# Kernel optimization log

Hardware: AMD Instinct MI355X
Metric: run time of the kernel (lower is better)

The kernel has to match this reference:

```python
import jax, jax.numpy as jnp
import numpy as np

N = 50000   # nodes
E = 600000  # edges (time_feat is per-edge: same mask indexes k and src_idx)
D = 128     # adapter_dim
C = 8       # num_clusters
SCALE = D ** -0.5


def setup_inputs() -> dict:
    key = jax.random.key(0)
    ks = jax.random.split(key, 12)
    s = 1.0 / np.sqrt(D)
    return {
        "node_feat": jax.random.normal(ks[0], (N, D), jnp.float32),
        "time_feat": jax.random.normal(ks[1], (E, D), jnp.float32),
        "context_feat": jax.random.normal(ks[2], (N, D), jnp.float32),
        "edge_index": jax.random.randint(ks[3], (2, E), 0, N),
        "Wq": jax.random.uniform(ks[4], (D, D), jnp.float32, -s, s),
        "bq": jnp.zeros((D,), jnp.float32),
        "Wk": jax.random.uniform(ks[5], (D, D), jnp.float32, -s, s),
        "bk": jnp.zeros((D,), jnp.float32),
        "Wv": jax.random.uniform(ks[6], (D, D), jnp.float32, -s, s),
        "bv": jnp.zeros((D,), jnp.float32),
        "cluster_emb": jax.random.normal(ks[7], (C, D), jnp.float32),
        "Wo": jax.random.uniform(ks[8], (D, D), jnp.float32, -s, s),
        "bo": jnp.zeros((D,), jnp.float32),
    }


def reference(node_feat, time_feat, context_feat, edge_index,
              Wq, bq, Wk, bk, Wv, bv, cluster_emb, Wo, bo):
    q = node_feat @ Wq + bq            # [N, D]
    k = time_feat @ Wk + bk            # [E, D]
    v = time_feat @ Wv + bv            # [E, D]

    # cluster routing: argmax(softmax(sim)) == argmax(sim)
    sim = (time_feat @ cluster_emb.T) * SCALE   # [E, C]
    assign = jnp.argmax(sim, axis=-1)           # [E] int

    src = edge_index[0]                          # [E]
    seg = assign * N + src                       # combined (cluster, dst-of-scatter) segment id
    nseg = C * N

    attn = jnp.sum(q[src] * k, axis=-1) * SCALE  # [E]

    # scatter_softmax per (cluster, src node)
    seg_max = jax.ops.segment_max(attn, seg, num_segments=nseg)
    ex = jnp.exp(attn - seg_max[seg])
    denom = jax.ops.segment_sum(ex, seg, num_segments=nseg)
    w = ex / denom[seg]                          # [E]

    # scatter_mean per (cluster, src node) -> [C, N, D]
    wv = v * w[:, None]
    sums = jax.ops.segment_sum(wv, seg, num_segments=nseg)                 # [C*N, D]
    counts = jax.ops.segment_sum(jnp.ones((E,), v.dtype), seg, num_segments=nseg)
    means = sums / jnp.maximum(counts, 1.0)[:, None]                       # empty -> 0
    per_cluster = means.reshape(C, N, D)

    # sum(outputs) / len(outputs): only non-empty clusters contribute an entry
    edges_per_cluster = jax.ops.segment_sum(jnp.ones((E,), jnp.float32), assign, num_segments=C)
    num_nonempty = jnp.sum((edges_per_cluster > 0).astype(jnp.float32))
    combined = per_cluster.sum(axis=0) / num_nonempty                      # [N, D]

    return jax.nn.relu(combined @ Wo + bo)
```

## Files before the change

### kernel.cpp

```cpp
#include <hip/hip_runtime.h>
#include <math.h>


#define NN 50000
#define NE 600000
#define DD 128
#define NC 8
#define SCALEF 0.08838834764831845f

#define OFF_DENOM    0
#define OFF_CNTSEG   400000
#define OFF_NODECNT  800000
#define OFF_FILL     850000
#define OFF_HIST     900000
#define ZERO_ELEMS   900016
#define OFF_NODEOFF  900016
#define OFF_PARTIAL  950016
#define OFF_INVNNE   950272
#define OFF_C0       950276
#define OFF_BQK      950528
#define OFF_BVO      950656
#define OFF_WQBK     950784
#define OFF_WQK      950912
#define OFF_WVO      967296
#define OFF_QB       983680
#define OFF_EX       1033680
#define OFF_ASSIGN   1633680
#define OFF_SORTED   2233680
#define OFF_SW       2833680
#define OFF_P        2883680

__global__ __launch_bounds__(128) void k_pre(
    const float* __restrict__ Wq, const float* __restrict__ bq,
    const float* __restrict__ Wk, const float* __restrict__ bk,
    const float* __restrict__ Wv, const float* __restrict__ bv,
    const float* __restrict__ Wo,
    float* __restrict__ Wqk, float* __restrict__ bqk,
    float* __restrict__ Wvo, float* __restrict__ bvo,
    float* __restrict__ wqbk, float* __restrict__ c0) {
  __shared__ float rq[DD], rv[DD];
  int b = blockIdx.x, i = threadIdx.x;
  if (b < DD) {
    rq[i] = Wq[b * DD + i];
    rv[i] = Wv[b * DD + i];
    __syncthreads();
    float aq = 0.f, av = 0.f;
    for (int j = 0; j < DD; j++) {
      aq += rq[j] * Wk[i * DD + j];
      av += rv[j] * Wo[j * DD + i];
    }
    Wqk[b * DD + i] = aq;
    Wvo[b * DD + i] = av;
  } else {
    float a1 = 0.f, a2 = 0.f, a3 = 0.f;
    for (int j = 0; j < DD; j++) {
      a1 += bq[j] * Wk[i * DD + j];
      a2 += bv[j] * Wo[j * DD + i];
      a3 += Wq[i * DD + j] * bk[j];
    }
    bqk[i] = a1; bvo[i] = a2; wqbk[i] = a3;
    if (i == 0) {
      float s = 0.f;
      for (int j = 0; j < DD; j++) s += bq[j] * bk[j];
      *c0 = s;
    }
  }
}

__global__ __launch_bounds__(256) void k_p(
    const float* __restrict__ nf, const float* __restrict__ Wqk,
    const float* __restrict__ bqk, const float* __restrict__ wqbk,
    const float* __restrict__ c0p,
    float* __restrict__ p, float* __restrict__ qb) {
  __shared__ float a_lds[64 * DD];
  __shared__ float wb_lds[DD];
  int t = threadIdx.x;
  long row0 = (long)blockIdx.x * 64;
  for (int it = 0; it < 8; it++) {
    int idx = (it * 256 + t) * 4;
    long r = row0 + idx / DD;
    float4 v = {0.f, 0.f, 0.f, 0.f};
    if (r < NN) v = *(const float4*)(nf + r * DD + (idx % DD));
    *(float4*)(a_lds + idx) = v;
  }
  if (t < DD) wb_lds[t] = wqbk[t];
  __syncthreads();
  int cg = t % 32, rg = t / 32;
  int col0 = cg * 4, r0 = rg * 8;
  float acc[8][4]; float qacc[8];
  for (int r = 0; r < 8; r++) { qacc[r] = 0.f; for (int c = 0; c < 4; c++) acc[r][c] = 0.f; }
  for (int k = 0; k < DD; k++) {
    float4 b4 = *(const float4*)(Wqk + k * DD + col0);
    float wbk = wb_lds[k];
    for (int r = 0; r < 8; r++) {
      float a = a_lds[(r0 + r) * DD + k];
      acc[r][0] += a * b4.x; acc[r][1] += a * b4.y;
      acc[r][2] += a * b4.z; acc[r][3] += a * b4.w;
      qacc[r] += a * wbk;
    }
  }
  float4 bq4 = *(const float4*)(bqk + col0);
  float c0v = *c0p;
  for (int r = 0; r < 8; r++) {
    long row = row0 + r0 + r;
    if (row < NN) {
      float4 o;
      o.x = acc[r][0] + bq4.x; o.y = acc[r][1] + bq4.y;
      o.z = acc[r][2] + bq4.z; o.w = acc[r][3] + bq4.w;
      *(float4*)(p + row * DD + col0) = o;
      if (cg == 0) qb[row] = qacc[r] + c0v;
    }
  }
}

__global__ __launch_bounds__(256) void k_edge1(
    const float* __restrict__ tf, const int* __restrict__ ei,
    const float* __restrict__ ce, const float* __restrict__ p,
    const float* __restrict__ qb,
    float* __restrict__ denom, int* __restrict__ cnt_seg,
    int* __restrict__ node_cnt, int* __restrict__ hist,
    float* __restrict__ exv, int* __restrict__ assign) {
  __shared__ float ce_lds[NC * DD];
  __shared__ int lhist[NC];
  int t = threadIdx.x;
  if (t < NC) lhist[t] = 0;
  *(float4*)(ce_lds + t * 4) = *(const float4*)(ce + t * 4);
  __syncthreads();

  int el = t >> 2, j = t & 3;
  long e = (long)blockIdx.x * 64 + el;
  const float* trow = tf + e * DD;
  float4 tv[8];
  for (int i = 0; i < 8; i++) tv[i] = *(const float4*)(trow + i * 16 + j * 4);
  int src = ei[e];

  float sims[NC];
  for (int c = 0; c < NC; c++) {
    const float* cr = ce_lds + c * DD;
    float s = 0.f;
    for (int i = 0; i < 8; i++) {
      float4 cv = *(const float4*)(cr + i * 16 + j * 4);
      s += tv[i].x * cv.x + tv[i].y * cv.y + tv[i].z * cv.z + tv[i].w * cv.w;
    }
    sims[c] = s;
  }
  for (int c = 0; c < NC; c++) {
    sims[c] += __shfl_xor(sims[c], 1);
    sims[c] += __shfl_xor(sims[c], 2);
  }
  float best = sims[0]; int bc = 0;
  for (int c = 1; c < NC; c++) if (sims[c] > best) { best = sims[c]; bc = c; }

  const float* prow = p + (long)src * DD;
  float a = 0.f;
  for (int i = 0; i < 8; i++) {
    float4 pv = *(const float4*)(prow + i * 16 + j * 4);
    a += tv[i].x * pv.x + tv[i].y * pv.y + tv[i].z * pv.z + tv[i].w * pv.w;
  }
  a += __shfl_xor(a, 1);
  a += __shfl_xor(a, 2);
  float attn = (a + qb[src]) * SCALEF;
  float ex = expf(attn);

  if (j == 0) {
    exv[e] = ex;
    assign[e] = bc;
    int seg = bc * NN + src;
    atomicAdd(&denom[seg], ex);
    atomicAdd(&cnt_seg[seg], 1);
    atomicAdd(&node_cnt[src], 1);
    atomicAdd(&lhist[bc], 1);
  }
  __syncthreads();
  if (t < NC) atomicAdd(&hist[t], lhist[t]);
}

__global__ __launch_bounds__(256) void k_scan1(const int* __restrict__ node_cnt,
                                               int* __restrict__ partial) {
  int i = blockIdx.x * 256 + threadIdx.x;
  int v = (i < NN) ? node_cnt[i] : 0;
  for (int o = 1; o < 64; o <<= 1) v += __shfl_xor(v, o);
  __shared__ int wsum[4];
  if ((threadIdx.x & 63) == 0) wsum[threadIdx.x >> 6] = v;
  __syncthreads();
  if (threadIdx.x == 0) partial[blockIdx.x] = wsum[0] + wsum[1] + wsum[2] + wsum[3];
}

__global__ __launch_bounds__(256) void k_scan2(int* __restrict__ partial,
                                               const int* __restrict__ hist,
                                               float* __restrict__ inv_nne) {
  __shared__ int s[256];
  int t = threadIdx.x;
  int v = (t < 196) ? partial[t] : 0;
  s[t] = v;
  __syncthreads();
  for (int o = 1; o < 256; o <<= 1) {
    int add = (t >= o) ? s[t - o] : 0;
    __syncthreads();
    s[t] += add;
    __syncthreads();
  }
  if (t < 196) partial[t] = s[t] - v;
  if (t == 0) {
    int nne = 0;
    for (int c = 0; c < NC; c++) nne += (hist[c] > 0) ? 1 : 0;
    *inv_nne = 1.0f / (float)(nne > 0 ? nne : 1);
  }
}

__global__ __launch_bounds__(256) void k_scan3(const int* __restrict__ node_cnt,
                                               const int* __restrict__ partial,
                                               int* __restrict__ node_off) {
  __shared__ int s[256];
  int t = threadIdx.x;
  int i = blockIdx.x * 256 + t;
  int v = (i < NN) ? node_cnt[i] : 0;
  s[t] = v;
  __syncthreads();
  for (int o = 1; o < 256; o <<= 1) {
    int add = (t >= o) ? s[t - o] : 0;
    __syncthreads();
    s[t] += add;
    __syncthreads();
  }
  if (i < NN) node_off[i] = partial[blockIdx.x] + s[t] - v;
}

__global__ __launch_bounds__(256) void k_scatter(const int* __restrict__ ei,
                                                 const int* __restrict__ node_off,
                                                 int* __restrict__ fill,
                                                 int* __restrict__ sorted) {
  long e = (long)blockIdx.x * 256 + threadIdx.x;
  if (e < NE) {
    int s = ei[e];
    int pos = node_off[s] + atomicAdd(&fill[s], 1);
    sorted[pos] = (int)e;
  }
}

__global__ __launch_bounds__(256) void k_edge2(
    const float* __restrict__ tf, const int* __restrict__ sorted,
    const int* __restrict__ node_off, const int* __restrict__ node_cnt,
    const int* __restrict__ assign, const float* __restrict__ exv,
    const float* __restrict__ denom, const int* __restrict__ cnt_seg,
    float* __restrict__ agg, float* __restrict__ sw) {
  int wave = threadIdx.x >> 6, lane = threadIdx.x & 63;
  int n = blockIdx.x * 4 + wave;
  int off = node_off[n], cnt = node_cnt[n];
  float a0 = 0.f, a1 = 0.f, swa = 0.f;
  for (int base = 0; base < cnt; base += 64) {
    int m = cnt - base; if (m > 64) m = 64;
    int e_l = 0; float s_l = 0.f;
    if (lane < m) {
      e_l = sorted[off + base + lane];
      int c = assign[e_l];
      int seg = c * NN + n;
      s_l = exv[e_l] / (denom[seg] * (float)cnt_seg[seg]);
    }
    for (int ii = 0; ii < m; ii++) {
      int e = __shfl(e_l, ii);
      float s = __shfl(s_l, ii);
      float2 tv = *(const float2*)(tf + (long)e * DD + lane * 2);
      a0 += s * tv.x; a1 += s * tv.y; swa += s;
    }
  }
  float2 o; o.x = a0; o.y = a1;
  *(float2*)(agg + (long)n * DD + lane * 2) = o;
  if (lane == 0) sw[n] = swa;
}

__global__ __launch_bounds__(256) void k_out(
    const float* __restrict__ agg, const float* __restrict__ Wvo,
    const float* __restrict__ bvo, const float* __restrict__ sw,
    const float* __restrict__ bo, const float* __restrict__ inv_nne,
    float* __restrict__ out) {
  __shared__ float a_lds[64 * DD];
  __shared__ float sw_lds[64];
  int t = threadIdx.x;
  long row0 = (long)blockIdx.x * 64;
  for (int it = 0; it < 8; it++) {
    int idx = (it * 256 + t) * 4;
    long r = row0 + idx / DD;
    float4 v = {0.f, 0.f, 0.f, 0.f};
    if (r < NN) v = *(const float4*)(agg + r * DD + (idx % DD));
    *(float4*)(a_lds + idx) = v;
  }
  if (t < 64) {
    long r = row0 + t;
    sw_lds[t] = (r < NN) ? sw[r] : 0.f;
  }
  __syncthreads();
  int cg = t % 32, rg = t / 32;
  int col0 = cg * 4, r0 = rg * 8;
  float acc[8][4];
  for (int r = 0; r < 8; r++) for (int c = 0; c < 4; c++) acc[r][c] = 0.f;
  for (int k = 0; k < DD; k++) {
    float4 b4 = *(const float4*)(Wvo + k * DD + col0);
    for (int r = 0; r < 8; r++) {
      float a = a_lds[(r0 + r) * DD + k];
      acc[r][0] += a * b4.x; acc[r][1] += a * b4.y;
      acc[r][2] += a * b4.z; acc[r][3] += a * b4.w;
    }
  }
  float4 bv4 = *(const float4*)(bvo + col0);
  float4 bo4 = *(const float4*)(bo + col0);
  float inv = *inv_nne;
  for (int r = 0; r < 8; r++) {
    long row = row0 + r0 + r;
    if (row < NN) {
      float s = sw_lds[r0 + r];
      float4 o;
      o.x = fmaxf((acc[r][0] + s * bv4.x) * inv + bo4.x, 0.f);
      o.y = fmaxf((acc[r][1] + s * bv4.y) * inv + bo4.y, 0.f);
      o.z = fmaxf((acc[r][2] + s * bv4.z) * inv + bo4.z, 0.f);
      o.w = fmaxf((acc[r][3] + s * bv4.w) * inv + bo4.w, 0.f);
      *(float4*)(out + row * DD + col0) = o;
    }
  }
}

extern "C" void kernel_launch(void* const* d_in, const int* in_sizes, int n_in,
                              void* d_out, int out_size, void* d_ws, size_t ws_size,
                              hipStream_t stream) {
  const float* nf = (const float*)d_in[0];
  const float* tf = (const float*)d_in[1];
  const int*   ei = (const int*)d_in[3];
  const float* Wq = (const float*)d_in[4];
  const float* bq = (const float*)d_in[5];
  const float* Wk = (const float*)d_in[6];
  const float* bk = (const float*)d_in[7];
  const float* Wv = (const float*)d_in[8];
  const float* bv = (const float*)d_in[9];
  const float* ce = (const float*)d_in[10];
  const float* Wo = (const float*)d_in[11];
  const float* bo = (const float*)d_in[12];
  float* out = (float*)d_out;

  float* ws  = (float*)d_ws;
  float* denom    = ws + OFF_DENOM;
  int*   cnt_seg  = (int*)(ws + OFF_CNTSEG);
  int*   node_cnt = (int*)(ws + OFF_NODECNT);
  int*   fill     = (int*)(ws + OFF_FILL);
  int*   hist     = (int*)(ws + OFF_HIST);
  int*   node_off = (int*)(ws + OFF_NODEOFF);
  int*   partial  = (int*)(ws + OFF_PARTIAL);
  float* inv_nne  = ws + OFF_INVNNE;
  float* c0       = ws + OFF_C0;
  float* bqk      = ws + OFF_BQK;
  float* bvo      = ws + OFF_BVO;
  float* wqbk     = ws + OFF_WQBK;
  float* Wqk      = ws + OFF_WQK;
  float* Wvo      = ws + OFF_WVO;
  float* qb       = ws + OFF_QB;
  float* exv      = ws + OFF_EX;
  int*   assign   = (int*)(ws + OFF_ASSIGN);
  int*   sorted   = (int*)(ws + OFF_SORTED);
  float* sw       = ws + OFF_SW;
  float* p        = ws + OFF_P;
  float* agg      = ws + OFF_P;

  hipMemsetAsync(d_ws, 0, (size_t)ZERO_ELEMS * 4, stream);

  k_pre<<<129, 128, 0, stream>>>(Wq, bq, Wk, bk, Wv, bv, Wo, Wqk, bqk, Wvo, bvo, wqbk, c0);
  k_p<<<(NN + 63) / 64, 256, 0, stream>>>(nf, Wqk, bqk, wqbk, c0, p, qb);
  k_edge1<<<NE / 64, 256, 0, stream>>>(tf, ei, ce, p, qb, denom, cnt_seg, node_cnt,
                                       hist, exv, assign);
  k_scan1<<<196, 256, 0, stream>>>(node_cnt, partial);
  k_scan2<<<1, 256, 0, stream>>>(partial, hist, inv_nne);
  k_scan3<<<196, 256, 0, stream>>>(node_cnt, partial, node_off);
  k_scatter<<<(NE + 255) / 256, 256, 0, stream>>>(ei, node_off, fill, sorted);
  k_edge2<<<NN / 4, 256, 0, stream>>>(tf, sorted, node_off, node_cnt, assign, exv,
                                      denom, cnt_seg, agg, sw);
  k_out<<<(NN + 63) / 64, 256, 0, stream>>>(agg, Wvo, bvo, sw, bo, inv_nne, out);
}
```

Measured before the change: 720.2 us.

## Fuse edge scoring into per-node aggregation kernel with LDS-staged time features

Removes the separate per-edge scoring kernel and its global atomics on per-segment denominators and counts. Each node's block now stages its incident time_feat rows in LDS, computes cluster assignment and attention there, and reduces denominators and counts in shared memory. The result is reused for the weighted aggregation, so time_feat is read once instead of twice. Node-degree counting moves into the weight-precompute launch, and the non-empty-cluster count becomes a bitmask OR. The cost is one block per node (50000 blocks) with a slower two-pass chunked path for nodes above 48 edges.

```diff
diff --git a/kernel.cpp b/kernel.cpp
--- a/kernel.cpp
+++ b/kernel.cpp
@@ -6,63 +6,71 @@
 #define NE 600000
 #define DD 128
 #define NC 8
+#define CAP 48
 #define SCALEF 0.08838834764831845f
 
-#define OFF_DENOM    0
-#define OFF_CNTSEG   400000
-#define OFF_NODECNT  800000
-#define OFF_FILL     850000
-#define OFF_HIST     900000
-#define ZERO_ELEMS   900016
-#define OFF_NODEOFF  900016
-#define OFF_PARTIAL  950016
-#define OFF_INVNNE   950272
-#define OFF_C0       950276
-#define OFF_BQK      950528
-#define OFF_BVO      950656
-#define OFF_WQBK     950784
-#define OFF_WQK      950912
-#define OFF_WVO      967296
-#define OFF_QB       983680
-#define OFF_EX       1033680
-#define OFF_ASSIGN   1633680
-#define OFF_SORTED   2233680
-#define OFF_SW       2833680
-#define OFF_P        2883680
-
-__global__ __launch_bounds__(128) void k_pre(
+#define OFF_NODECNT  0
+#define OFF_FILL     50000
+#define OFF_MASK     100000
+#define ZERO_ELEMS   100256
+#define OFF_NODEOFF  100352
+#define OFF_PARTIAL  150352
+#define OFF_BQK      150608
+#define OFF_BVO      150736
+#define OFF_WQBK     150864
+#define OFF_C0       150992
+#define OFF_WQK      151008
+#define OFF_WVO      167392
+#define OFF_QB       183776
+#define OFF_SORTED   233776
+#define OFF_SW       833776
+#define OFF_EXV      883776
+#define OFF_ASSIGN   1483776
+#define OFF_P        2083776
+
+__global__ __launch_bounds__(256) void k_pre_count(
     const float* __restrict__ Wq, const float* __restrict__ bq,
     const float* __restrict__ Wk, const float* __restrict__ bk,
     const float* __restrict__ Wv, const float* __restrict__ bv,
-    const float* __restrict__ Wo,
+    const float* __restrict__ Wo, const int* __restrict__ ei,
+    int* __restrict__ node_cnt,
     float* __restrict__ Wqk, float* __restrict__ bqk,
     float* __restrict__ Wvo, float* __restrict__ bvo,
     float* __restrict__ wqbk, float* __restrict__ c0) {
+  int bid = blockIdx.x, t = threadIdx.x;
+  if (bid >= 129) {
+    long e = (long)(bid - 129) * 256 + t;
+    if (e < NE) atomicAdd(&node_cnt[ei[e]], 1);
+    return;
+  }
   __shared__ float rq[DD], rv[DD];
-  int b = blockIdx.x, i = threadIdx.x;
+  int b = bid;
   if (b < DD) {
-    rq[i] = Wq[b * DD + i];
-    rv[i] = Wv[b * DD + i];
-    __syncthreads();
-    float aq = 0.f, av = 0.f;
-    for (int j = 0; j < DD; j++) {
-      aq += rq[j] * Wk[i * DD + j];
-      av += rv[j] * Wo[j * DD + i];
-    }
-    Wqk[b * DD + i] = aq;
-    Wvo[b * DD + i] = av;
+    if (t < DD) { rq[t] = Wq[b * DD + t]; rv[t] = Wv[b * DD + t]; }
+    __syncthreads();
+    if (t < DD) {
+      float aq = 0.f, av = 0.f;
+      for (int j = 0; j < DD; j++) {
+        aq += rq[j] * Wk[t * DD + j];
+        av += rv[j] * Wo[j * DD + t];
+      }
+      Wqk[b * DD + t] = aq;
+      Wvo[b * DD + t] = av;
+    }
   } else {
-    float a1 = 0.f, a2 = 0.f, a3 = 0.f;
-    for (int j = 0; j < DD; j++) {
-      a1 += bq[j] * Wk[i * DD + j];
-      a2 += bv[j] * Wo[j * DD + i];
-      a3 += Wq[i * DD + j] * bk[j];
-    }
-    bqk[i] = a1; bvo[i] = a2; wqbk[i] = a3;
-    if (i == 0) {
-      float s = 0.f;
-      for (int j = 0; j < DD; j++) s += bq[j] * bk[j];
-      *c0 = s;
+    if (t < DD) {
+      float a1 = 0.f, a2 = 0.f, a3 = 0.f;
+      for (int j = 0; j < DD; j++) {
+        a1 += bq[j] * Wk[t * DD + j];
+        a2 += bv[j] * Wo[j * DD + t];
+        a3 += Wq[t * DD + j] * bk[j];
+      }
+      bqk[t] = a1; bvo[t] = a2; wqbk[t] = a3;
+      if (t == 0) {
+        float s = 0.f;
+        for (int j = 0; j < DD; j++) s += bq[j] * bk[j];
+        *c0 = s;
+      }
     }
   }
 }
@@ -113,68 +121,6 @@
   }
 }
 
-__global__ __launch_bounds__(256) void k_edge1(
-    const float* __restrict__ tf, const int* __restrict__ ei,
-    const float* __restrict__ ce, const float* __restrict__ p,
-    const float* __restrict__ qb,
-    float* __restrict__ denom, int* __restrict__ cnt_seg,
-    int* __restrict__ node_cnt, int* __restrict__ hist,
-    float* __restrict__ exv, int* __restrict__ assign) {
-  __shared__ float ce_lds[NC * DD];
-  __shared__ int lhist[NC];
-  int t = threadIdx.x;
-  if (t < NC) lhist[t] = 0;
-  *(float4*)(ce_lds + t * 4) = *(const float4*)(ce + t * 4);
-  __syncthreads();
-
-  int el = t >> 2, j = t & 3;
-  long e = (long)blockIdx.x * 64 + el;
-  const float* trow = tf + e * DD;
-  float4 tv[8];
-  for (int i = 0; i < 8; i++) tv[i] = *(const float4*)(trow + i * 16 + j * 4);
-  int src = ei[e];
-
-  float sims[NC];
-  for (int c = 0; c < NC; c++) {
-    const float* cr = ce_lds + c * DD;
-    float s = 0.f;
-    for (int i = 0; i < 8; i++) {
-      float4 cv = *(const float4*)(cr + i * 16 + j * 4);
-      s += tv[i].x * cv.x + tv[i].y * cv.y + tv[i].z * cv.z + tv[i].w * cv.w;
-    }
-    sims[c] = s;
-  }
-  for (int c = 0; c < NC; c++) {
-    sims[c] += __shfl_xor(sims[c], 1);
-    sims[c] += __shfl_xor(sims[c], 2);
-  }
-  float best = sims[0]; int bc = 0;
-  for (int c = 1; c < NC; c++) if (sims[c] > best) { best = sims[c]; bc = c; }
-
-  const float* prow = p + (long)src * DD;
-  float a = 0.f;
-  for (int i = 0; i < 8; i++) {
-    float4 pv = *(const float4*)(prow + i * 16 + j * 4);
-    a += tv[i].x * pv.x + tv[i].y * pv.y + tv[i].z * pv.z + tv[i].w * pv.w;
-  }
-  a += __shfl_xor(a, 1);
-  a += __shfl_xor(a, 2);
-  float attn = (a + qb[src]) * SCALEF;
-  float ex = expf(attn);
-
-  if (j == 0) {
-    exv[e] = ex;
-    assign[e] = bc;
-    int seg = bc * NN + src;
-    atomicAdd(&denom[seg], ex);
-    atomicAdd(&cnt_seg[seg], 1);
-    atomicAdd(&node_cnt[src], 1);
-    atomicAdd(&lhist[bc], 1);
-  }
-  __syncthreads();
-  if (t < NC) atomicAdd(&hist[t], lhist[t]);
-}
-
 __global__ __launch_bounds__(256) void k_scan1(const int* __restrict__ node_cnt,
                                                int* __restrict__ partial) {
   int i = blockIdx.x * 256 + threadIdx.x;
@@ -186,9 +132,7 @@
   if (threadIdx.x == 0) partial[blockIdx.x] = wsum[0] + wsum[1] + wsum[2] + wsum[3];
 }
 
-__global__ __launch_bounds__(256) void k_scan2(int* __restrict__ partial,
-                                               const int* __restrict__ hist,
-                                               float* __restrict__ inv_nne) {
+__global__ __launch_bounds__(256) void k_scan2(int* __restrict__ partial) {
   __shared__ int s[256];
   int t = threadIdx.x;
   int v = (t < 196) ? partial[t] : 0;
@@ -201,11 +145,6 @@
     __syncthreads();
   }
   if (t < 196) partial[t] = s[t] - v;
-  if (t == 0) {
-    int nne = 0;
-    for (int c = 0; c < NC; c++) nne += (hist[c] > 0) ? 1 : 0;
-    *inv_nne = 1.0f / (float)(nne > 0 ? nne : 1);
-  }
 }
 
 __global__ __launch_bounds__(256) void k_scan3(const int* __restrict__ node_cnt,
@@ -238,45 +177,186 @@
   }
 }
 
-__global__ __launch_bounds__(256) void k_edge2(
+__device__ __forceinline__ void sim_attn_edge(
+    const float* t_lds, const float* ce_lds, const float* p_lds, float qbv,
+    int el, int j, float& ex_out, int& bc_out) {
+  const float* trow = t_lds + el * DD;
+  int sw8 = el & 7;
+  float4 tv[8];
+  for (int i = 0; i < 8; i++)
+    tv[i] = *(const float4*)(trow + ((i * 4 + j) ^ sw8) * 4);
+  float sims[NC];
+  for (int c = 0; c < NC; c++) {
+    const float* cr = ce_lds + c * DD;
+    float s = 0.f;
+    for (int i = 0; i < 8; i++) {
+      float4 cv = *(const float4*)(cr + (i * 4 + j) * 4);
+      s += tv[i].x * cv.x + tv[i].y * cv.y + tv[i].z * cv.z + tv[i].w * cv.w;
+    }
+    sims[c] = s;
+  }
+  float a = 0.f;
+  for (int i = 0; i < 8; i++) {
+    float4 pv = *(const float4*)(p_lds + (i * 4 + j) * 4);
+    a += tv[i].x * pv.x + tv[i].y * pv.y + tv[i].z * pv.z + tv[i].w * pv.w;
+  }
+  for (int c = 0; c < NC; c++) {
+    sims[c] += __shfl_xor(sims[c], 1);
+    sims[c] += __shfl_xor(sims[c], 2);
+  }
+  a += __shfl_xor(a, 1);
+  a += __shfl_xor(a, 2);
+  float best = sims[0]; int bc = 0;
+  for (int c = 1; c < NC; c++) if (sims[c] > best) { best = sims[c]; bc = c; }
+  ex_out = expf((a + qbv) * SCALEF);
+  bc_out = bc;
+}
+
+__global__ __launch_bounds__(256) void k_fused(
     const float* __restrict__ tf, const int* __restrict__ sorted,
     const int* __restrict__ node_off, const int* __restrict__ node_cnt,
-    const int* __restrict__ assign, const float* __restrict__ exv,
-    const float* __restrict__ denom, const int* __restrict__ cnt_seg,
+    const float* __restrict__ ce, const float* __restrict__ p,
+    const float* __restrict__ qb,
+    float* __restrict__ exv_g, int* __restrict__ assign_g,
+    int* __restrict__ maskArr,
     float* __restrict__ agg, float* __restrict__ sw) {
-  int wave = threadIdx.x >> 6, lane = threadIdx.x & 63;
-  int n = blockIdx.x * 4 + wave;
+  __shared__ float t_lds[CAP * DD];
+  __shared__ float ce_lds[NC * DD];
+  __shared__ float p_lds[DD];
+  __shared__ float team_lds[DD];
+  __shared__ float exf[CAP];
+  __shared__ float scl[CAP];
+  __shared__ int   cli[CAP];
+  __shared__ int   eidx[CAP];
+  __shared__ float D_sh[NC];
+  __shared__ int   C_sh[NC];
+  __shared__ float qb_sh;
+
+  int n = blockIdx.x;
+  int t = threadIdx.x;
   int off = node_off[n], cnt = node_cnt[n];
-  float a0 = 0.f, a1 = 0.f, swa = 0.f;
-  for (int base = 0; base < cnt; base += 64) {
-    int m = cnt - base; if (m > 64) m = 64;
-    int e_l = 0; float s_l = 0.f;
-    if (lane < m) {
-      e_l = sorted[off + base + lane];
-      int c = assign[e_l];
-      int seg = c * NN + n;
-      s_l = exv[e_l] / (denom[seg] * (float)cnt_seg[seg]);
-    }
-    for (int ii = 0; ii < m; ii++) {
-      int e = __shfl(e_l, ii);
-      float s = __shfl(s_l, ii);
-      float2 tv = *(const float2*)(tf + (long)e * DD + lane * 2);
-      a0 += s * tv.x; a1 += s * tv.y; swa += s;
-    }
-  }
-  float2 o; o.x = a0; o.y = a1;
-  *(float2*)(agg + (long)n * DD + lane * 2) = o;
-  if (lane == 0) sw[n] = swa;
+
+  if (cnt == 0) {
+    if (t < 32) {
+      float4 z = {0.f, 0.f, 0.f, 0.f};
+      *(float4*)(agg + (long)n * DD + t * 4) = z;
+    }
+    if (t == 0) sw[n] = 0.f;
+    return;
+  }
+
+  *(float4*)(ce_lds + t * 4) = *(const float4*)(ce + t * 4);
+  if (t < 32) *(float4*)(p_lds + t * 4) = *(const float4*)(p + (long)n * DD + t * 4);
+  if (t < NC) { D_sh[t] = 0.f; C_sh[t] = 0; }
+  if (t == 0) qb_sh = qb[n];
+
+  int el = t >> 2, j = t & 3;
+  int d = t & 127, team = t >> 7;
+  float aggacc = 0.f;
+
+  if (cnt <= CAP) {
+    if (t < cnt) eidx[t] = sorted[off + t];
+    __syncthreads();
+    int total4 = cnt * 32;
+    for (int i = t; i < total4; i += 256) {
+      int e_i = i >> 5, d4 = i & 31;
+      *(float4*)(t_lds + e_i * DD + (d4 ^ (e_i & 7)) * 4) =
+          *(const float4*)(tf + (long)eidx[e_i] * DD + d4 * 4);
+    }
+    __syncthreads();
+    if (el < cnt) {
+      float ex; int bc;
+      sim_attn_edge(t_lds, ce_lds, p_lds, qb_sh, el, j, ex, bc);
+      if (j == 0) {
+        exf[el] = ex; cli[el] = bc;
+        atomicAdd(&D_sh[bc], ex);
+        atomicAdd(&C_sh[bc], 1);
+      }
+    }
+    __syncthreads();
+    if (t < cnt) scl[t] = exf[t] / (D_sh[cli[t]] * (float)C_sh[cli[t]]);
+    if (t == 0) {
+      int m = 0; float s = 0.f;
+      for (int c = 0; c < NC; c++)
+        if (C_sh[c] > 0) { m |= 1 << c; s += 1.0f / (float)C_sh[c]; }
+      atomicOr(&maskArr[n & 255], m);
+      sw[n] = s;
+    }
+    __syncthreads();
+    for (int e = team; e < cnt; e += 2)
+      aggacc += scl[e] * t_lds[e * DD + (((d >> 2) ^ (e & 7)) << 2) + (d & 3)];
+  } else {
+    int nchunk = (cnt + CAP - 1) / CAP;
+    for (int ch = 0; ch < nchunk; ch++) {
+      int base = ch * CAP;
+      int m = cnt - base; if (m > CAP) m = CAP;
+      __syncthreads();
+      if (t < m) eidx[t] = sorted[off + base + t];
+      __syncthreads();
+      int total4 = m * 32;
+      for (int i = t; i < total4; i += 256) {
+        int e_i = i >> 5, d4 = i & 31;
+        *(float4*)(t_lds + e_i * DD + (d4 ^ (e_i & 7)) * 4) =
+            *(const float4*)(tf + (long)eidx[e_i] * DD + d4 * 4);
+      }
+      __syncthreads();
+      if (el < m) {
+        float ex; int bc;
+        sim_attn_edge(t_lds, ce_lds, p_lds, qb_sh, el, j, ex, bc);
+        if (j == 0) {
+          exv_g[off + base + el] = ex;
+          assign_g[off + base + el] = bc;
+          atomicAdd(&D_sh[bc], ex);
+          atomicAdd(&C_sh[bc], 1);
+        }
+      }
+    }
+    __syncthreads();
+    if (t == 0) {
+      int m = 0; float s = 0.f;
+      for (int c = 0; c < NC; c++)
+        if (C_sh[c] > 0) { m |= 1 << c; s += 1.0f / (float)C_sh[c]; }
+      atomicOr(&maskArr[n & 255], m);
+      sw[n] = s;
+    }
+    for (int ch = 0; ch < nchunk; ch++) {
+      int base = ch * CAP;
+      int m = cnt - base; if (m > CAP) m = CAP;
+      __syncthreads();
+      if (t < m) {
+        eidx[t] = sorted[off + base + t];
+        int c = assign_g[off + base + t];
+        scl[t] = exv_g[off + base + t] / (D_sh[c] * (float)C_sh[c]);
+      }
+      __syncthreads();
+      int total4 = m * 32;
+      for (int i = t; i < total4; i += 256) {
+        int e_i = i >> 5, d4 = i & 31;
+        *(float4*)(t_lds + e_i * DD + (d4 ^ (e_i & 7)) * 4) =
+            *(const float4*)(tf + (long)eidx[e_i] * DD + d4 * 4);
+      }
+      __syncthreads();
+      for (int e = team; e < m; e += 2)
+        aggacc += scl[e] * t_lds[e * DD + (((d >> 2) ^ (e & 7)) << 2) + (d & 3)];
+    }
+  }
+  if (team == 1) team_lds[d] = aggacc;
+  __syncthreads();
+  if (team == 0) agg[(long)n * DD + d] = aggacc + team_lds[d];
 }
 
 __global__ __launch_bounds__(256) void k_out(
     const float* __restrict__ agg, const float* __restrict__ Wvo,
     const float* __restrict__ bvo, const float* __restrict__ sw,
-    const float* __restrict__ bo, const float* __restrict__ inv_nne,
+    const float* __restrict__ bo, const int* __restrict__ maskArr,
     float* __restrict__ out) {
   __shared__ float a_lds[64 * DD];
   __shared__ float sw_lds[64];
+  __shared__ int morw[4];
   int t = threadIdx.x;
+  int mv = maskArr[t];
+  for (int o = 1; o < 64; o <<= 1) mv |= __shfl_xor(mv, o);
+  if ((t & 63) == 0) morw[t >> 6] = mv;
   long row0 = (long)blockIdx.x * 64;
   for (int it = 0; it < 8; it++) {
     int idx = (it * 256 + t) * 4;
@@ -290,6 +370,9 @@
     sw_lds[t] = (r < NN) ? sw[r] : 0.f;
   }
   __syncthreads();
+  int full = morw[0] | morw[1] | morw[2] | morw[3];
+  int nne = __popc(full); if (nne == 0) nne = 1;
+  float inv = 1.0f / (float)nne;
   int cg = t % 32, rg = t / 32;
   int col0 = cg * 4, r0 = rg * 8;
   float acc[8][4];
@@ -304,7 +387,6 @@
   }
   float4 bv4 = *(const float4*)(bvo + col0);
   float4 bo4 = *(const float4*)(bo + col0);
-  float inv = *inv_nne;
   for (int r = 0; r < 8; r++) {
     long row = row0 + r0 + r;
     if (row < NN) {
@@ -337,39 +419,35 @@
   float* out = (float*)d_out;
 
   float* ws  = (float*)d_ws;
-  float* denom    = ws + OFF_DENOM;
-  int*   cnt_seg  = (int*)(ws + OFF_CNTSEG);
   int*   node_cnt = (int*)(ws + OFF_NODECNT);
   int*   fill     = (int*)(ws + OFF_FILL);
-  int*   hist     = (int*)(ws + OFF_HIST);
+  int*   maskArr  = (int*)(ws + OFF_MASK);
   int*   node_off = (int*)(ws + OFF_NODEOFF);
   int*   partial  = (int*)(ws + OFF_PARTIAL);
-  float* inv_nne  = ws + OFF_INVNNE;
-  float* c0       = ws + OFF_C0;
   float* bqk      = ws + OFF_BQK;
   float* bvo      = ws + OFF_BVO;
   float* wqbk     = ws + OFF_WQBK;
+  float* c0       = ws + OFF_C0;
   float* Wqk      = ws + OFF_WQK;
   float* Wvo      = ws + OFF_WVO;
   float* qb       = ws + OFF_QB;
-  float* exv      = ws + OFF_EX;
-  int*   assign   = (int*)(ws + OFF_ASSIGN);
   int*   sorted   = (int*)(ws + OFF_SORTED);
   float* sw       = ws + OFF_SW;
+  float* exv      = ws + OFF_EXV;
+  int*   assign   = (int*)(ws + OFF_ASSIGN);
   float* p        = ws + OFF_P;
   float* agg      = ws + OFF_P;
 
   hipMemsetAsync(d_ws, 0, (size_t)ZERO_ELEMS * 4, stream);
 
-  k_pre<<<129, 128, 0, stream>>>(Wq, bq, Wk, bk, Wv, bv, Wo, Wqk, bqk, Wvo, bvo, wqbk, c0);
+  k_pre_count<<<129 + (NE + 255) / 256, 256, 0, stream>>>(
+      Wq, bq, Wk, bk, Wv, bv, Wo, ei, node_cnt, Wqk, bqk, Wvo, bvo, wqbk, c0);
   k_p<<<(NN + 63) / 64, 256, 0, stream>>>(nf, Wqk, bqk, wqbk, c0, p, qb);
-  k_edge1<<<NE / 64, 256, 0, stream>>>(tf, ei, ce, p, qb, denom, cnt_seg, node_cnt,
-                                       hist, exv, assign);
   k_scan1<<<196, 256, 0, stream>>>(node_cnt, partial);
-  k_scan2<<<1, 256, 0, stream>>>(partial, hist, inv_nne);
+  k_scan2<<<1, 256, 0, stream>>>(partial);
   k_scan3<<<196, 256, 0, stream>>>(node_cnt, partial, node_off);
   k_scatter<<<(NE + 255) / 256, 256, 0, stream>>>(ei, node_off, fill, sorted);
-  k_edge2<<<NN / 4, 256, 0, stream>>>(tf, sorted, node_off, node_cnt, assign, exv,
-                                      denom, cnt_seg, agg, sw);
-  k_out<<<(NN + 63) / 64, 256, 0, stream>>>(agg, Wvo, bvo, sw, bo, inv_nne, out);
-}
+  k_fused<<<NN, 256, 0, stream>>>(tf, sorted, node_off, node_cnt, ce, p, qb,
+                                  exv, assign, maskArr, agg, sw);
+  k_out<<<(NN + 63) / 64, 256, 0, stream>>>(agg, Wvo, bvo, sw, bo, maskArr, out);
+}
```

Result: slower. 805.0 us (+11.8%).
